# Kernel tuning notes

Hardware: AMD Instinct MI355X
Metric: run time of the kernel (lower is better)

Reference implementation:

```python
import jax, jax.numpy as jnp
import numpy as np

N_NODES = 100000
N_EDGES = 3200000
NEG_SLOPE = 0.2  # PyG GATConv default


def setup_inputs() -> dict:
    key = jax.random.key(0)
    ks = jax.random.split(key, 10)
    g = 0.1
    return {
        "x": jax.random.normal(ks[0], (N_NODES, 3), jnp.float32),
        "edge_index": jax.random.randint(ks[1], (2, N_EDGES), 0, N_NODES),
        "w1": jax.random.normal(ks[2], (3, 32), jnp.float32) * g,
        "att_src1": jax.random.normal(ks[3], (2, 16), jnp.float32) * g,
        "att_dst1": jax.random.normal(ks[4], (2, 16), jnp.float32) * g,
        "b1": jnp.zeros((32,), jnp.float32),
        "w2": jax.random.normal(ks[5], (32, 14), jnp.float32) * g,
        "att_src2": jax.random.normal(ks[6], (2, 7), jnp.float32) * g,
        "att_dst2": jax.random.normal(ks[7], (2, 7), jnp.float32) * g,
        "b2": jnp.zeros((7,), jnp.float32),
    }


def _gat_conv(x, src, dst, W, att_src, att_dst, bias, heads, out_ch, concat, n):
    # x: [N, F_in]; src/dst: [E] (self-loops already appended)
    xl = (x @ W).reshape(n, heads, out_ch)          # [N, H, C]
    a_s = jnp.sum(xl * att_src[None], axis=-1)      # [N, H]
    a_d = jnp.sum(xl * att_dst[None], axis=-1)      # [N, H]
    alpha = jax.nn.leaky_relu(a_s[src] + a_d[dst], NEG_SLOPE)  # [E, H]
    # segment softmax over edges sharing a destination node
    mx = jax.ops.segment_max(alpha, dst, num_segments=n)        # [N, H]
    e = jnp.exp(alpha - mx[dst])
    denom = jax.ops.segment_sum(e, dst, num_segments=n)         # [N, H]
    alpha = e / (denom[dst] + 1e-16)
    msg = xl[src] * alpha[:, :, None]                            # [E, H, C]
    out = jax.ops.segment_sum(msg, dst, num_segments=n)         # [N, H, C]
    out = out.reshape(n, heads * out_ch) if concat else out.mean(axis=1)
    return out + bias


def reference(x, edge_index, w1, att_src1, att_dst1, b1, w2, att_src2, att_dst2, b2):
    n = x.shape[0]
    loop = jnp.arange(n)
    src = jnp.concatenate([edge_index[0], loop])  # add self-loops (PyG default)
    dst = jnp.concatenate([edge_index[1], loop])
    h = _gat_conv(x, src, dst, w1, att_src1, att_dst1, b1, 2, 16, True, n)
    h = jax.nn.relu(h)
    h = _gat_conv(h, src, dst, w2, att_src2, att_dst2, b2, 2, 7, False, n)
    return jax.nn.log_softmax(h, axis=1)
```

## Files before the change

### kernel.cpp

```cpp
#include <hip/hip_runtime.h>
#include <hip/hip_fp16.h>

static constexpr float NEG_SLOPE = 0.2f;
#define BUCKET_BITS 6
#define BNODES (1 << BUCKET_BITS)
#define MAXNB 2048
#define MAXSUP 32
#define SUPER_SHIFT 12
#define CHUNK1 2048
#define CHUNK 4096
#define PTHREADS 256
#define STHREADS 128
#define SORT_CAP 3072
#define SK(i) ((i) + ((i) >> 5))

__device__ __forceinline__ float2 h2f(float r) {
  return __half22float2(__builtin_bit_cast(__half2, r));
}

__global__ void k_node1(const float* __restrict__ x,
                        const float* __restrict__ w1,
                        const float* __restrict__ atts,
                        const float* __restrict__ attd,
                        float4* __restrict__ xp,
                        float* __restrict__ ad_,
                        unsigned* __restrict__ scur,
                        unsigned* __restrict__ bcur,
                        int n) {
  int i = blockIdx.x * blockDim.x + threadIdx.x;
  if (i < MAXSUP) scur[i] = 0u;
  if (i < MAXNB) bcur[i] = 0u;
  if (i >= n) return;
  float x0 = x[3*i], x1 = x[3*i+1], x2 = x[3*i+2];
  float v[32];
#pragma unroll
  for (int j = 0; j < 32; ++j)
    v[j] = fmaf(x0, w1[j], fmaf(x1, w1[32+j], x2 * w1[64+j]));
  float s0=0.f, s1=0.f, d0=0.f, d1=0.f;
#pragma unroll
  for (int k = 0; k < 16; ++k) {
    s0 = fmaf(v[k],    atts[k],    s0);
    d0 = fmaf(v[k],    attd[k],    d0);
    s1 = fmaf(v[16+k], atts[16+k], s1);
    d1 = fmaf(v[16+k], attd[16+k], d1);
  }
  float4 r;
  r.x = __builtin_bit_cast(float, __floats2half2_rn(x0, x1));
  r.y = __builtin_bit_cast(float, __floats2half2_rn(x2, s0));
  r.z = __builtin_bit_cast(float, __floats2half2_rn(s1, 0.f));
  r.w = 0.f;
  xp[i] = r;
  ad_[2*i] = d0; ad_[2*i+1] = d1;
}

__global__ void k_part1(const int* __restrict__ esrc, const int* __restrict__ edst,
                        unsigned* __restrict__ scur, unsigned* __restrict__ tmp1,
                        unsigned caps, int E) {
  __shared__ unsigned whist[4 * MAXSUP], wsub[4 * MAXSUP], woffs[4 * MAXSUP];
  int t = threadIdx.x;
  int w = t >> 6;
  for (int i = t; i < 4 * MAXSUP; i += PTHREADS) { whist[i] = 0u; woffs[i] = 0u; }
  __syncthreads();
  int e0 = blockIdx.x * CHUNK1;
  int e1 = min(E, e0 + CHUNK1);
  unsigned pkr[8], hir[8];
  int eb = e0 + t;
#pragma unroll
  for (int k = 0; k < 8; ++k) {
    int e = eb + k * PTHREADS;
    if (e < e1) {
      unsigned d = (unsigned)edst[e];
      unsigned s = (unsigned)esrc[e];
      unsigned hi = d >> SUPER_SHIFT;
      pkr[k] = (((d >> BUCKET_BITS) & 63u) << 24)
             | ((d & (BNODES - 1u)) << 17) | s;
      hir[k] = hi;
      atomicAdd(&whist[w * MAXSUP + hi], 1u);
    } else {
      hir[k] = 0xFFFFFFFFu;
    }
  }
  __syncthreads();
  if (t < MAXSUP) {
    unsigned h0 = whist[t],             h1 = whist[MAXSUP + t];
    unsigned h2 = whist[2*MAXSUP + t],  h3 = whist[3*MAXSUP + t];
    unsigned tot = h0 + h1 + h2 + h3;
    unsigned base = tot ? atomicAdd(&scur[t], tot) : 0u;
    wsub[t]            = base;
    wsub[MAXSUP + t]   = base + h0;
    wsub[2*MAXSUP + t] = base + h0 + h1;
    wsub[3*MAXSUP + t] = base + h0 + h1 + h2;
  }
  __syncthreads();
#pragma unroll
  for (int k = 0; k < 8; ++k) {
    unsigned hi = hir[k];
    if (hi != 0xFFFFFFFFu) {
      unsigned r = atomicAdd(&woffs[w * MAXSUP + hi], 1u);
      tmp1[(size_t)hi * caps + wsub[w * MAXSUP + hi] + r] = pkr[k];
    }
  }
}

__global__ void k_part2(const unsigned* __restrict__ tmp1,
                        const unsigned* __restrict__ scnt,
                        unsigned* __restrict__ bcur,
                        unsigned* __restrict__ packed2,
                        unsigned caps, unsigned capb, int maxch, int nb) {
  __shared__ unsigned stage[CHUNK];
  __shared__ unsigned hist[64], base[64], offs[64];
  int s = blockIdx.x / maxch;
  int c = blockIdx.x % maxch;
  unsigned count = scnt[s];
  int e0 = c * CHUNK;
  if ((unsigned)e0 >= count) return;
  int e1 = min((int)count, e0 + CHUNK);
  int t = threadIdx.x;
  if (t < 64) { hist[t] = 0u; offs[t] = 0u; }
  __syncthreads();
  const unsigned* src = tmp1 + (size_t)s * caps;
  for (int i = e0 + t; i < e1; i += PTHREADS) {
    unsigned pk = src[i];
    atomicAdd(&hist[pk >> 24], 1u);
    stage[i - e0] = pk;
  }
  __syncthreads();
  if (t < 64) {
    unsigned b = ((unsigned)s << 6) | (unsigned)t;
    if (hist[t] && b < (unsigned)nb) base[t] = atomicAdd(&bcur[b], hist[t]);
  }
  __syncthreads();
  for (int i = e0 + t; i < e1; i += PTHREADS) {
    unsigned pk = stage[i - e0];
    unsigned idx = pk >> 24;
    unsigned r = atomicAdd(&offs[idx], 1u);
    unsigned pos = base[idx] + r;
    unsigned b = ((unsigned)s << 6) | idx;
    if (pos < capb)
      packed2[(size_t)b * capb + pos] = pk & 0x00FFFFFFu;
  }
}

__global__ void k_sortb_g1(const unsigned* __restrict__ bcnt,
                           const unsigned* __restrict__ packed2,
                           const float4* __restrict__ xp,
                           const float* __restrict__ x,
                           const float* __restrict__ ad_,
                           const float* __restrict__ w1,
                           const float* __restrict__ atts1,
                           const float* __restrict__ b1,
                           const float* __restrict__ w2,
                           const float* __restrict__ atts2,
                           const float* __restrict__ attd2,
                           int* __restrict__ col,
                           unsigned* __restrict__ rp,
                           unsigned* __restrict__ rend,
                           float4* __restrict__ xl2p,
                           float* __restrict__ ad2,
                           unsigned capb, int n) {
  __shared__ unsigned stage_out[SORT_CAP + SORT_CAP / 32];
  __shared__ unsigned cnt[BNODES], excl[BNODES], off[BNODES];
  int b = blockIdx.x;
  int size = (int)min(bcnt[b], capb);
  size_t bin = (size_t)b * capb;
  const unsigned* src = packed2 + bin;
  int base = b << BUCKET_BITS;
  int nNodes = min(BNODES, n - base);
  int t = threadIdx.x;
  if (t < BNODES) cnt[t] = 0u;
  __syncthreads();
  for (int i = t; i < size; i += STHREADS)
    atomicAdd(&cnt[(src[i] >> 17) & 63u], 1u);
  __syncthreads();
  if (t < BNODES) {
    unsigned v = cnt[t];
    unsigned s = v;
#pragma unroll
    for (int o2 = 1; o2 < 64; o2 <<= 1) {
      unsigned u = (unsigned)__shfl_up((int)s, o2, 64);
      if (t >= o2) s += u;
    }
    unsigned e = s - v;
    excl[t] = e; off[t] = e;
  }
  __syncthreads();
  for (int i = t; i < size; i += STHREADS) {
    unsigned pk = src[i];
    unsigned slot = atomicAdd(&off[(pk >> 17) & 63u], 1u);
    stage_out[SK(slot)] = pk & 0x1FFFFu;
  }
  __syncthreads();
  for (int i = t; i < size; i += STHREADS) col[bin + i] = (int)stage_out[SK(i)];
  if (t < nNodes) {
    unsigned r0 = (unsigned)bin + excl[t];
    rp[base + t] = r0;
    rend[base + t] = r0 + cnt[t];
  }
  int node = t >> 1, h = t & 1;
  if (node >= nNodes) return;
  int gnode = base + node;
  float adh = ad_[(size_t)gnode * 2 + h];
  unsigned kb = excl[node], ke = kb + cnt[node];
  float4 acc = make_float4(0.f, 0.f, 0.f, 0.f);
  auto procr = [&](float4 r) {
    float2 fx01 = h2f(r.x);
    float2 fx2s = h2f(r.y);
    float2 fs1  = h2f(r.z);
    float as = h ? fs1.x : fx2s.y;
    float a = as + adh; a = (a >= 0.f) ? a : NEG_SLOPE * a;
    float e = __expf(a);
    acc.x = fmaf(fx01.x, e, acc.x);
    acc.y = fmaf(fx01.y, e, acc.y);
    acc.z = fmaf(fx2s.x, e, acc.z);
    acc.w += e;
  };
  unsigned k = kb;
  for (; k + 8 <= ke; k += 8) {
    unsigned i0 = stage_out[SK(k)],   i1 = stage_out[SK(k+1)];
    unsigned i2 = stage_out[SK(k+2)], i3 = stage_out[SK(k+3)];
    unsigned i4 = stage_out[SK(k+4)], i5 = stage_out[SK(k+5)];
    unsigned i6 = stage_out[SK(k+6)], i7 = stage_out[SK(k+7)];
    float4 r0 = xp[i0], r1 = xp[i1], r2 = xp[i2], r3 = xp[i3];
    float4 r4 = xp[i4], r5 = xp[i5], r6 = xp[i6], r7 = xp[i7];
    procr(r0); procr(r1); procr(r2); procr(r3);
    procr(r4); procr(r5); procr(r6); procr(r7);
  }
  for (; k < ke; ++k) procr(xp[stage_out[SK(k)]]);
  float x0 = x[3*gnode], x1 = x[3*gnode+1], x2 = x[3*gnode+2];
  int cb = h << 4;
  float v[16];
#pragma unroll
  for (int j = 0; j < 16; ++j)
    v[j] = fmaf(x0, w1[cb+j], fmaf(x1, w1[32+cb+j], x2 * w1[64+cb+j]));
  float sh = 0.f;
#pragma unroll
  for (int kk = 0; kk < 16; ++kk) sh = fmaf(v[kk], atts1[cb+kk], sh);
  float ah = sh + adh;
  ah = (ah >= 0.f) ? ah : NEG_SLOPE * ah;
  float eh = __expf(ah);
  float inv = 1.f / (acc.w + eh + 1e-16f);
  float hbuf[16];
#pragma unroll
  for (int j = 0; j < 16; ++j) {
    float nm = fmaf(acc.x, w1[cb+j],
               fmaf(acc.y, w1[32+cb+j],
               fmaf(acc.z, w1[64+cb+j], eh * v[j])));
    float tv = nm * inv + b1[cb+j];
    hbuf[j] = tv > 0.f ? tv : 0.f;
  }
  float o[14];
#pragma unroll
  for (int j = 0; j < 14; ++j) o[j] = 0.f;
#pragma unroll
  for (int ch = 0; ch < 16; ++ch) {
#pragma unroll
    for (int j = 0; j < 14; ++j)
      o[j] = fmaf(hbuf[ch], w2[14*(cb+ch) + j], o[j]);
  }
#pragma unroll
  for (int j = 0; j < 14; ++j)
    o[j] += __shfl_xor(o[j], 1, 2);
  int ob = 7 * h;
  float th = 0.f, dh2 = 0.f;
#pragma unroll
  for (int kk = 0; kk < 7; ++kk) {
    th  = fmaf(o[ob+kk], atts2[ob+kk], th);
    dh2 = fmaf(o[ob+kk], attd2[ob+kk], dh2);
  }
  float4 rr;
  rr.x = __builtin_bit_cast(float, __floats2half2_rn(o[ob+0], o[ob+1]));
  rr.y = __builtin_bit_cast(float, __floats2half2_rn(o[ob+2], o[ob+3]));
  rr.z = __builtin_bit_cast(float, __floats2half2_rn(o[ob+4], o[ob+5]));
  rr.w = __builtin_bit_cast(float, __floats2half2_rn(o[ob+6], th));
  xl2p[(size_t)gnode * 2 + h] = rr;
  ad2[(size_t)gnode * 2 + h] = dh2;
}

__global__ void k_gather_final(const unsigned* __restrict__ rp,
                               const unsigned* __restrict__ rend,
                               const int* __restrict__ col,
                               const float4* __restrict__ xl2p,
                               const float* __restrict__ ad2,
                               const float* __restrict__ b2,
                               float* __restrict__ out,
                               int n) {
  int idx = blockIdx.x * blockDim.x + threadIdx.x;
  int d = idx >> 1;
  int h = idx & 1;
  if (d >= n) return;
  float adh = ad2[2*d + h];
  float acc[7] = {0.f,0.f,0.f,0.f,0.f,0.f,0.f};
  float den = 0.f;

  auto proc = [&](float4 r) {
    float2 c01 = h2f(r.x), c23 = h2f(r.y), c45 = h2f(r.z), c6a = h2f(r.w);
    float a = c6a.y + adh; a = (a >= 0.f) ? a : NEG_SLOPE*a;
    float e = __expf(a);
    acc[0] = fmaf(c01.x, e, acc[0]); acc[1] = fmaf(c01.y, e, acc[1]);
    acc[2] = fmaf(c23.x, e, acc[2]); acc[3] = fmaf(c23.y, e, acc[3]);
    acc[4] = fmaf(c45.x, e, acc[4]); acc[5] = fmaf(c45.y, e, acc[5]);
    acc[6] = fmaf(c6a.x, e, acc[6]); den += e;
  };

  unsigned jb = rp[d];
  unsigned je = rend[d];
  unsigned j = jb;
  for (; j + 8 <= je; j += 8) {
    int s0 = col[j],   s1 = col[j+1], s2 = col[j+2], s3 = col[j+3];
    int s4 = col[j+4], s5 = col[j+5], s6 = col[j+6], s7 = col[j+7];
    float4 r0 = xl2p[2*(size_t)s0 + h];
    float4 r1 = xl2p[2*(size_t)s1 + h];
    float4 r2 = xl2p[2*(size_t)s2 + h];
    float4 r3 = xl2p[2*(size_t)s3 + h];
    float4 r4 = xl2p[2*(size_t)s4 + h];
    float4 r5 = xl2p[2*(size_t)s5 + h];
    float4 r6 = xl2p[2*(size_t)s6 + h];
    float4 r7 = xl2p[2*(size_t)s7 + h];
    proc(r0); proc(r1); proc(r2); proc(r3);
    proc(r4); proc(r5); proc(r6); proc(r7);
  }
  for (; j < je; ++j) proc(xl2p[2*(size_t)col[j] + h]);
  proc(xl2p[2*(size_t)d + h]);

  float inv = 1.f / (den + 1e-16f);
  float v[7];
#pragma unroll
  for (int c = 0; c < 7; ++c) {
    float mine = acc[c] * inv;
    float other = __shfl_xor(mine, 1, 2);
    v[c] = 0.5f * (mine + other) + b2[c];
  }
  float m = v[0];
#pragma unroll
  for (int c = 1; c < 7; ++c) m = fmaxf(m, v[c]);
  float s = 0.f;
#pragma unroll
  for (int c = 0; c < 7; ++c) s += __expf(v[c] - m);
  float ls = __logf(s);
  float* o = out + (size_t)d * 7;
  if (h == 0) {
    o[0] = v[0]-m-ls; o[1] = v[1]-m-ls; o[2] = v[2]-m-ls; o[3] = v[3]-m-ls;
  } else {
    o[4] = v[4]-m-ls; o[5] = v[5]-m-ls; o[6] = v[6]-m-ls;
  }
}

extern "C" void kernel_launch(void* const* d_in, const int* in_sizes, int n_in,
                              void* d_out, int out_size, void* d_ws, size_t ws_size,
                              hipStream_t stream) {
  const float* x    = (const float*)d_in[0];
  const int*   ei   = (const int*)  d_in[1];
  const float* w1   = (const float*)d_in[2];
  const float* as1w = (const float*)d_in[3];
  const float* ad1w = (const float*)d_in[4];
  const float* b1   = (const float*)d_in[5];
  const float* w2   = (const float*)d_in[6];
  const float* as2w = (const float*)d_in[7];
  const float* ad2w = (const float*)d_in[8];
  const float* b2   = (const float*)d_in[9];
  float* out = (float*)d_out;

  const int n = in_sizes[0] / 3;
  const int E = in_sizes[1] / 2;
  const int* esrc = ei;
  const int* edst = ei + E;
  const int nb   = (n + BNODES - 1) >> BUCKET_BITS;
  const int nsup = (n + (1 << SUPER_SHIFT) - 1) >> SUPER_SHIFT;

  const unsigned avgb = (unsigned)(E / nb);
  const unsigned capb = (avgb + avgb / 16 + 384 + 7u) & ~7u;
  const unsigned avgs = (unsigned)(E / nsup);
  const unsigned caps = avgs + avgs / 16 + 4096;
  const int maxch = (int)((caps + CHUNK - 1) / CHUNK);

  const size_t Na = ((size_t)n + 3) & ~(size_t)3;
  float* ws = (float*)d_ws;
  float4* xp    = (float4*)ws;
  float*  ad1   = ws + 4*Na;
  float4* xl2p  = (float4*)(ws + 6*Na);
  float*  ad2   = ws + 14*Na;
  unsigned* ctrl   = (unsigned*)(ws + 16*Na);
  unsigned* scur   = ctrl;
  unsigned* bcur   = ctrl + MAXSUP;
  unsigned* rp     = bcur + MAXNB;
  unsigned* rend   = rp + Na;
  unsigned* packed2= rend + Na;
  int*      col    = (int*)(packed2 + (size_t)nb * capb);
  unsigned* tmp1   = (unsigned*)(col + (size_t)nb * capb);

  const int nbN = (n + 255) / 256;
  const int nbC1 = (E + CHUNK1 - 1) / CHUNK1;

  k_node1<<<nbN, 256, 0, stream>>>(x, w1, as1w, ad1w, xp, ad1, scur, bcur, n);

  k_part1<<<nbC1, PTHREADS, 0, stream>>>(esrc, edst, scur, tmp1, caps, E);
  k_part2<<<nsup * maxch, PTHREADS, 0, stream>>>(tmp1, scur, bcur, packed2,
                                                 caps, capb, maxch, nb);

  k_sortb_g1<<<nb, STHREADS, 0, stream>>>(bcur, packed2, xp, x, ad1, w1, as1w,
                                          b1, w2, as2w, ad2w, col, rp, rend,
                                          xl2p, ad2, capb, n);

  k_gather_final<<<(2*n + 255)/256, 256, 0, stream>>>(
      rp, rend, col, xl2p, ad2, b2, out, n);
}
```

Before: 132.2 us.

## Replace per-bucket CSR sort with LDS fixed-point atomic accumulation in both layers

Measured after the change: 116.0 us. 1.14x faster.

```diff
diff --git a/kernel.cpp b/kernel.cpp
--- a/kernel.cpp
+++ b/kernel.cpp
@@ -10,13 +10,16 @@
 #define CHUNK1 2048
 #define CHUNK 4096
 #define PTHREADS 256
-#define STHREADS 128
-#define SORT_CAP 3072
-#define SK(i) ((i) + ((i) >> 5))
+#define SCALE1 262144.0f
+#define INV_SCALE1 (1.0f / 262144.0f)
+#define SCALE2 131072.0f
+#define INV_SCALE2 (1.0f / 131072.0f)
 
 __device__ __forceinline__ float2 h2f(float r) {
   return __half22float2(__builtin_bit_cast(__half2, r));
 }
+__device__ __forceinline__ int f2i1(float v) { return __float2int_rn(v * SCALE1); }
+__device__ __forceinline__ int f2i2(float v) { return __float2int_rn(v * SCALE2); }
 
 __global__ void k_node1(const float* __restrict__ x,
                         const float* __restrict__ w1,
@@ -141,91 +144,59 @@
   }
 }
 
-__global__ void k_sortb_g1(const unsigned* __restrict__ bcnt,
-                           const unsigned* __restrict__ packed2,
-                           const float4* __restrict__ xp,
-                           const float* __restrict__ x,
-                           const float* __restrict__ ad_,
-                           const float* __restrict__ w1,
-                           const float* __restrict__ atts1,
-                           const float* __restrict__ b1,
-                           const float* __restrict__ w2,
-                           const float* __restrict__ atts2,
-                           const float* __restrict__ attd2,
-                           int* __restrict__ col,
-                           unsigned* __restrict__ rp,
-                           unsigned* __restrict__ rend,
-                           float4* __restrict__ xl2p,
-                           float* __restrict__ ad2,
-                           unsigned capb, int n) {
-  __shared__ unsigned stage_out[SORT_CAP + SORT_CAP / 32];
-  __shared__ unsigned cnt[BNODES], excl[BNODES], off[BNODES];
+__global__ void k_bucketL1i(const unsigned* __restrict__ bcnt,
+                            const unsigned* __restrict__ packed2,
+                            const float4* __restrict__ xp,
+                            const float* __restrict__ x,
+                            const float* __restrict__ ad_,
+                            const float* __restrict__ w1,
+                            const float* __restrict__ atts1,
+                            const float* __restrict__ b1,
+                            const float* __restrict__ w2,
+                            const float* __restrict__ atts2,
+                            const float* __restrict__ attd2,
+                            float4* __restrict__ xl2p,
+                            float* __restrict__ ad2,
+                            unsigned capb, int n) {
+  __shared__ int acc[8 * BNODES];
+  __shared__ float adl[2 * BNODES];
   int b = blockIdx.x;
   int size = (int)min(bcnt[b], capb);
-  size_t bin = (size_t)b * capb;
-  const unsigned* src = packed2 + bin;
+  const unsigned* src = packed2 + (size_t)b * capb;
   int base = b << BUCKET_BITS;
   int nNodes = min(BNODES, n - base);
   int t = threadIdx.x;
-  if (t < BNODES) cnt[t] = 0u;
-  __syncthreads();
-  for (int i = t; i < size; i += STHREADS)
-    atomicAdd(&cnt[(src[i] >> 17) & 63u], 1u);
-  __syncthreads();
-  if (t < BNODES) {
-    unsigned v = cnt[t];
-    unsigned s = v;
-#pragma unroll
-    for (int o2 = 1; o2 < 64; o2 <<= 1) {
-      unsigned u = (unsigned)__shfl_up((int)s, o2, 64);
-      if (t >= o2) s += u;
-    }
-    unsigned e = s - v;
-    excl[t] = e; off[t] = e;
-  }
-  __syncthreads();
-  for (int i = t; i < size; i += STHREADS) {
+  for (int i = t; i < 8 * BNODES; i += PTHREADS) acc[i] = 0;
+  for (int i = t; i < nNodes * 2; i += PTHREADS) adl[i] = ad_[(size_t)base*2 + i];
+  __syncthreads();
+  for (int i = t; i < size; i += PTHREADS) {
     unsigned pk = src[i];
-    unsigned slot = atomicAdd(&off[(pk >> 17) & 63u], 1u);
-    stage_out[SK(slot)] = pk & 0x1FFFFu;
-  }
-  __syncthreads();
-  for (int i = t; i < size; i += STHREADS) col[bin + i] = (int)stage_out[SK(i)];
-  if (t < nNodes) {
-    unsigned r0 = (unsigned)bin + excl[t];
-    rp[base + t] = r0;
-    rend[base + t] = r0 + cnt[t];
-  }
+    unsigned s = pk & 0x1FFFFu;
+    unsigned local = (pk >> 17) & 63u;
+    float4 r = xp[s];
+    float2 x01 = h2f(r.x), x2s = h2f(r.y), s1v = h2f(r.z);
+    float a0 = x2s.y + adl[local*2];     a0 = (a0 >= 0.f) ? a0 : NEG_SLOPE*a0;
+    float a1 = s1v.x + adl[local*2+1];   a1 = (a1 >= 0.f) ? a1 : NEG_SLOPE*a1;
+    float e0 = __expf(a0), e1 = __expf(a1);
+    atomicAdd(&acc[0*BNODES + local], f2i1(x01.x * e0));
+    atomicAdd(&acc[1*BNODES + local], f2i1(x01.y * e0));
+    atomicAdd(&acc[2*BNODES + local], f2i1(x2s.x * e0));
+    atomicAdd(&acc[3*BNODES + local], f2i1(e0));
+    atomicAdd(&acc[4*BNODES + local], f2i1(x01.x * e1));
+    atomicAdd(&acc[5*BNODES + local], f2i1(x01.y * e1));
+    atomicAdd(&acc[6*BNODES + local], f2i1(x2s.x * e1));
+    atomicAdd(&acc[7*BNODES + local], f2i1(e1));
+  }
+  __syncthreads();
   int node = t >> 1, h = t & 1;
-  if (node >= nNodes) return;
+  if (node >= nNodes || t >= 2*BNODES) return;
   int gnode = base + node;
-  float adh = ad_[(size_t)gnode * 2 + h];
-  unsigned kb = excl[node], ke = kb + cnt[node];
-  float4 acc = make_float4(0.f, 0.f, 0.f, 0.f);
-  auto procr = [&](float4 r) {
-    float2 fx01 = h2f(r.x);
-    float2 fx2s = h2f(r.y);
-    float2 fs1  = h2f(r.z);
-    float as = h ? fs1.x : fx2s.y;
-    float a = as + adh; a = (a >= 0.f) ? a : NEG_SLOPE * a;
-    float e = __expf(a);
-    acc.x = fmaf(fx01.x, e, acc.x);
-    acc.y = fmaf(fx01.y, e, acc.y);
-    acc.z = fmaf(fx2s.x, e, acc.z);
-    acc.w += e;
-  };
-  unsigned k = kb;
-  for (; k + 8 <= ke; k += 8) {
-    unsigned i0 = stage_out[SK(k)],   i1 = stage_out[SK(k+1)];
-    unsigned i2 = stage_out[SK(k+2)], i3 = stage_out[SK(k+3)];
-    unsigned i4 = stage_out[SK(k+4)], i5 = stage_out[SK(k+5)];
-    unsigned i6 = stage_out[SK(k+6)], i7 = stage_out[SK(k+7)];
-    float4 r0 = xp[i0], r1 = xp[i1], r2 = xp[i2], r3 = xp[i3];
-    float4 r4 = xp[i4], r5 = xp[i5], r6 = xp[i6], r7 = xp[i7];
-    procr(r0); procr(r1); procr(r2); procr(r3);
-    procr(r4); procr(r5); procr(r6); procr(r7);
-  }
-  for (; k < ke; ++k) procr(xp[stage_out[SK(k)]]);
+  float adh = adl[node*2 + h];
+  int kb = h * 4;
+  float ax = (float)acc[(kb+0)*BNODES + node] * INV_SCALE1;
+  float ay = (float)acc[(kb+1)*BNODES + node] * INV_SCALE1;
+  float az = (float)acc[(kb+2)*BNODES + node] * INV_SCALE1;
+  float aw = (float)acc[(kb+3)*BNODES + node] * INV_SCALE1;
   float x0 = x[3*gnode], x1 = x[3*gnode+1], x2 = x[3*gnode+2];
   int cb = h << 4;
   float v[16];
@@ -238,13 +209,13 @@
   float ah = sh + adh;
   ah = (ah >= 0.f) ? ah : NEG_SLOPE * ah;
   float eh = __expf(ah);
-  float inv = 1.f / (acc.w + eh + 1e-16f);
+  float inv = 1.f / (aw + eh + 1e-16f);
   float hbuf[16];
 #pragma unroll
   for (int j = 0; j < 16; ++j) {
-    float nm = fmaf(acc.x, w1[cb+j],
-               fmaf(acc.y, w1[32+cb+j],
-               fmaf(acc.z, w1[64+cb+j], eh * v[j])));
+    float nm = fmaf(ax, w1[cb+j],
+               fmaf(ay, w1[32+cb+j],
+               fmaf(az, w1[64+cb+j], eh * v[j])));
     float tv = nm * inv + b1[cb+j];
     hbuf[j] = tv > 0.f ? tv : 0.f;
   }
@@ -276,73 +247,85 @@
   ad2[(size_t)gnode * 2 + h] = dh2;
 }
 
-__global__ void k_gather_final(const unsigned* __restrict__ rp,
-                               const unsigned* __restrict__ rend,
-                               const int* __restrict__ col,
-                               const float4* __restrict__ xl2p,
-                               const float* __restrict__ ad2,
-                               const float* __restrict__ b2,
-                               float* __restrict__ out,
-                               int n) {
-  int idx = blockIdx.x * blockDim.x + threadIdx.x;
-  int d = idx >> 1;
-  int h = idx & 1;
-  if (d >= n) return;
-  float adh = ad2[2*d + h];
-  float acc[7] = {0.f,0.f,0.f,0.f,0.f,0.f,0.f};
-  float den = 0.f;
-
-  auto proc = [&](float4 r) {
-    float2 c01 = h2f(r.x), c23 = h2f(r.y), c45 = h2f(r.z), c6a = h2f(r.w);
-    float a = c6a.y + adh; a = (a >= 0.f) ? a : NEG_SLOPE*a;
+__global__ void k_bucketL2i(const unsigned* __restrict__ bcnt,
+                            const unsigned* __restrict__ packed2,
+                            const float4* __restrict__ xl2p,
+                            const float* __restrict__ ad2,
+                            const float* __restrict__ b2,
+                            float* __restrict__ out,
+                            unsigned capb, int n) {
+  __shared__ int acc[16 * BNODES];
+  __shared__ float adl[2 * BNODES];
+  int b = blockIdx.x;
+  int size = (int)min(bcnt[b], capb);
+  const unsigned* src = packed2 + (size_t)b * capb;
+  int base = b << BUCKET_BITS;
+  int nNodes = min(BNODES, n - base);
+  int t = threadIdx.x;
+  for (int i = t; i < 16 * BNODES; i += PTHREADS) acc[i] = 0;
+  for (int i = t; i < nNodes * 2; i += PTHREADS) adl[i] = ad2[(size_t)base*2 + i];
+  __syncthreads();
+  for (int i = t; i < size; i += PTHREADS) {
+    unsigned pk = src[i];
+    unsigned s = pk & 0x1FFFFu;
+    unsigned local = (pk >> 17) & 63u;
+    float4 rA = xl2p[2*(size_t)s];
+    float4 rB = xl2p[2*(size_t)s + 1];
+    float2 c01 = h2f(rA.x), c23 = h2f(rA.y), c45 = h2f(rA.z), c6a = h2f(rA.w);
+    float a = c6a.y + adl[local*2]; a = (a >= 0.f) ? a : NEG_SLOPE*a;
     float e = __expf(a);
-    acc[0] = fmaf(c01.x, e, acc[0]); acc[1] = fmaf(c01.y, e, acc[1]);
-    acc[2] = fmaf(c23.x, e, acc[2]); acc[3] = fmaf(c23.y, e, acc[3]);
-    acc[4] = fmaf(c45.x, e, acc[4]); acc[5] = fmaf(c45.y, e, acc[5]);
-    acc[6] = fmaf(c6a.x, e, acc[6]); den += e;
-  };
-
-  unsigned jb = rp[d];
-  unsigned je = rend[d];
-  unsigned j = jb;
-  for (; j + 8 <= je; j += 8) {
-    int s0 = col[j],   s1 = col[j+1], s2 = col[j+2], s3 = col[j+3];
-    int s4 = col[j+4], s5 = col[j+5], s6 = col[j+6], s7 = col[j+7];
-    float4 r0 = xl2p[2*(size_t)s0 + h];
-    float4 r1 = xl2p[2*(size_t)s1 + h];
-    float4 r2 = xl2p[2*(size_t)s2 + h];
-    float4 r3 = xl2p[2*(size_t)s3 + h];
-    float4 r4 = xl2p[2*(size_t)s4 + h];
-    float4 r5 = xl2p[2*(size_t)s5 + h];
-    float4 r6 = xl2p[2*(size_t)s6 + h];
-    float4 r7 = xl2p[2*(size_t)s7 + h];
-    proc(r0); proc(r1); proc(r2); proc(r3);
-    proc(r4); proc(r5); proc(r6); proc(r7);
-  }
-  for (; j < je; ++j) proc(xl2p[2*(size_t)col[j] + h]);
-  proc(xl2p[2*(size_t)d + h]);
-
-  float inv = 1.f / (den + 1e-16f);
-  float v[7];
+    atomicAdd(&acc[0*BNODES + local], f2i2(c01.x * e));
+    atomicAdd(&acc[1*BNODES + local], f2i2(c01.y * e));
+    atomicAdd(&acc[2*BNODES + local], f2i2(c23.x * e));
+    atomicAdd(&acc[3*BNODES + local], f2i2(c23.y * e));
+    atomicAdd(&acc[4*BNODES + local], f2i2(c45.x * e));
+    atomicAdd(&acc[5*BNODES + local], f2i2(c45.y * e));
+    atomicAdd(&acc[6*BNODES + local], f2i2(c6a.x * e));
+    atomicAdd(&acc[7*BNODES + local], f2i2(e));
+    float2 d01 = h2f(rB.x), d23 = h2f(rB.y), d45 = h2f(rB.z), d6a = h2f(rB.w);
+    a = d6a.y + adl[local*2 + 1]; a = (a >= 0.f) ? a : NEG_SLOPE*a;
+    e = __expf(a);
+    atomicAdd(&acc[ 8*BNODES + local], f2i2(d01.x * e));
+    atomicAdd(&acc[ 9*BNODES + local], f2i2(d01.y * e));
+    atomicAdd(&acc[10*BNODES + local], f2i2(d23.x * e));
+    atomicAdd(&acc[11*BNODES + local], f2i2(d23.y * e));
+    atomicAdd(&acc[12*BNODES + local], f2i2(d45.x * e));
+    atomicAdd(&acc[13*BNODES + local], f2i2(d45.y * e));
+    atomicAdd(&acc[14*BNODES + local], f2i2(d6a.x * e));
+    atomicAdd(&acc[15*BNODES + local], f2i2(e));
+  }
+  __syncthreads();
+  if (t >= nNodes) return;
+  int gnode = base + t;
+  float4 rA = xl2p[2*(size_t)gnode];
+  float4 rB = xl2p[2*(size_t)gnode + 1];
+  float2 c01 = h2f(rA.x), c23 = h2f(rA.y), c45 = h2f(rA.z), c6a = h2f(rA.w);
+  float2 d01 = h2f(rB.x), d23 = h2f(rB.y), d45 = h2f(rB.z), d6a = h2f(rB.w);
+  float a0 = c6a.y + adl[t*2];     a0 = (a0 >= 0.f) ? a0 : NEG_SLOPE*a0;
+  float a1 = d6a.y + adl[t*2 + 1]; a1 = (a1 >= 0.f) ? a1 : NEG_SLOPE*a1;
+  float e0 = __expf(a0), e1 = __expf(a1);
+  float chA[7] = {c01.x, c01.y, c23.x, c23.y, c45.x, c45.y, c6a.x};
+  float chB[7] = {d01.x, d01.y, d23.x, d23.y, d45.x, d45.y, d6a.x};
+  float den0 = (float)acc[7*BNODES + t]  * INV_SCALE2 + e0 + 1e-16f;
+  float den1 = (float)acc[15*BNODES + t] * INV_SCALE2 + e1 + 1e-16f;
+  float inv0 = 1.f / den0, inv1 = 1.f / den1;
+  float vv[7];
 #pragma unroll
   for (int c = 0; c < 7; ++c) {
-    float mine = acc[c] * inv;
-    float other = __shfl_xor(mine, 1, 2);
-    v[c] = 0.5f * (mine + other) + b2[c];
-  }
-  float m = v[0];
-#pragma unroll
-  for (int c = 1; c < 7; ++c) m = fmaxf(m, v[c]);
-  float s = 0.f;
-#pragma unroll
-  for (int c = 0; c < 7; ++c) s += __expf(v[c] - m);
-  float ls = __logf(s);
-  float* o = out + (size_t)d * 7;
-  if (h == 0) {
-    o[0] = v[0]-m-ls; o[1] = v[1]-m-ls; o[2] = v[2]-m-ls; o[3] = v[3]-m-ls;
-  } else {
-    o[4] = v[4]-m-ls; o[5] = v[5]-m-ls; o[6] = v[6]-m-ls;
-  }
+    float h0 = ((float)acc[c*BNODES + t]       * INV_SCALE2 + chA[c] * e0) * inv0;
+    float h1 = ((float)acc[(8 + c)*BNODES + t] * INV_SCALE2 + chB[c] * e1) * inv1;
+    vv[c] = 0.5f * (h0 + h1) + b2[c];
+  }
+  float m = vv[0];
+#pragma unroll
+  for (int c = 1; c < 7; ++c) m = fmaxf(m, vv[c]);
+  float sum = 0.f;
+#pragma unroll
+  for (int c = 0; c < 7; ++c) sum += __expf(vv[c] - m);
+  float ls = __logf(sum);
+  float* o = out + (size_t)gnode * 7;
+#pragma unroll
+  for (int c = 0; c < 7; ++c) o[c] = vv[c] - m - ls;
 }
 
 extern "C" void kernel_launch(void* const* d_in, const int* in_sizes, int n_in,
@@ -382,11 +365,8 @@
   unsigned* ctrl   = (unsigned*)(ws + 16*Na);
   unsigned* scur   = ctrl;
   unsigned* bcur   = ctrl + MAXSUP;
-  unsigned* rp     = bcur + MAXNB;
-  unsigned* rend   = rp + Na;
-  unsigned* packed2= rend + Na;
-  int*      col    = (int*)(packed2 + (size_t)nb * capb);
-  unsigned* tmp1   = (unsigned*)(col + (size_t)nb * capb);
+  unsigned* packed2= bcur + MAXNB;
+  unsigned* tmp1   = packed2 + (size_t)nb * capb;
 
   const int nbN = (n + 255) / 256;
   const int nbC1 = (E + CHUNK1 - 1) / CHUNK1;
@@ -397,10 +377,10 @@
   k_part2<<<nsup * maxch, PTHREADS, 0, stream>>>(tmp1, scur, bcur, packed2,
                                                  caps, capb, maxch, nb);
 
-  k_sortb_g1<<<nb, STHREADS, 0, stream>>>(bcur, packed2, xp, x, ad1, w1, as1w,
-                                          b1, w2, as2w, ad2w, col, rp, rend,
-                                          xl2p, ad2, capb, n);
-
-  k_gather_final<<<(2*n + 255)/256, 256, 0, stream>>>(
-      rp, rend, col, xl2p, ad2, b2, out, n);
-}
+  k_bucketL1i<<<nb, PTHREADS, 0, stream>>>(bcur, packed2, xp, x, ad1, w1, as1w,
+                                           b1, w2, as2w, ad2w, xl2p, ad2,
+                                           capb, n);
+
+  k_bucketL2i<<<nb, PTHREADS, 0, stream>>>(bcur, packed2, xl2p, ad2, b2, out,
+                                           capb, n);
+}
```
